# Optimization experiments

Hardware: AMD Instinct MI355X
Metric: run time of the kernel (lower is better)

Reference implementation:

```python
import jax, jax.numpy as jnp
import numpy as np

E = 600000
N = 50000
H = 128
OE = 256


def swish(v):
    return v * jax.nn.sigmoid(v)


def setup_inputs() -> dict:
    key = jax.random.key(0)
    ks = jax.random.split(key, 16)
    inp = {
        "x": jax.random.normal(ks[0], (E, H), dtype=jnp.float32),
        "rbf": jax.random.normal(ks[1], (E, 6), dtype=jnp.float32),
        "i": jax.random.randint(ks[2], (E,), 0, N, dtype=jnp.int32),
        "edge_index": jax.random.randint(ks[3], (2, E), 0, N, dtype=jnp.int32),
        "edge_weight": jax.random.uniform(ks[4], (E,), dtype=jnp.float32),
        "batch": jax.random.randint(ks[5], (N,), 0, 32, dtype=jnp.int32),
        "num_nodes": N,
        "W_rbf": jax.random.normal(ks[6], (H, 6), dtype=jnp.float32) * 0.2,
        "W_up": jax.random.normal(ks[7], (OE, H), dtype=jnp.float32) * (1.0 / np.sqrt(H)),
        "b_up": jnp.zeros((OE,), dtype=jnp.float32),
        "W_l1": jax.random.normal(ks[8], (OE, OE), dtype=jnp.float32) * (1.0 / np.sqrt(OE)),
        "b_l1": jnp.zeros((OE,), dtype=jnp.float32),
        "W_l2": jax.random.normal(ks[9], (OE, OE), dtype=jnp.float32) * (1.0 / np.sqrt(OE)),
        "b_l2": jnp.zeros((OE,), dtype=jnp.float32),
        "W_l3": jax.random.normal(ks[10], (OE, OE), dtype=jnp.float32) * (1.0 / np.sqrt(OE)),
        "b_l3": jnp.zeros((OE,), dtype=jnp.float32),
        "W_out": jax.random.normal(ks[11], (1, OE), dtype=jnp.float32) * (1.0 / np.sqrt(OE)),
        "W_w": jax.random.normal(ks[12], (1, H), dtype=jnp.float32) * (1.0 / np.sqrt(H)),
        "b_w": jnp.zeros((1,), dtype=jnp.float32),
    }
    return inp


def reference(x, rbf, i, edge_index, edge_weight, batch, num_nodes,
              W_rbf, W_up, b_up, W_l1, b_l1, W_l2, b_l2, W_l3, b_l3,
              W_out, W_w, b_w):
    # edge_index / edge_weight are unused in the original forward.
    # x = lin_rbf(rbf) * x  -> [E, H]
    xe = (rbf @ W_rbf.T) * x
    # scatter-add edges -> nodes: [N, H]
    xn = jax.ops.segment_sum(xe, i, num_segments=num_nodes)
    # energy head: alpha = w_lin(x) before lin_up
    alpha = xn @ W_w.T + b_w  # [N, 1]
    x2 = xn @ W_up.T + b_up   # [N, OE]
    for W, b in ((W_l1, b_l1), (W_l2, b_l2), (W_l3, b_l3)):
        x2 = swish(x2 @ W.T + b)
    out = (x2 @ W_out.T) * alpha  # [N, 1]
    return (out, batch)
```

## Files before the change

kernel.cpp:

```cpp
#include <hip/hip_runtime.h>
#include <hip/hip_bf16.h>
#include <math.h>

#define E_CNT 600000
#define N_CNT 50000
#define H_DIM 128
#define OE_DIM 256

typedef __attribute__((ext_vector_type(8))) short short8;
typedef __attribute__((ext_vector_type(4))) float f32x4;

#define WS_EIDS   0
#define WS_OFF    2400000
#define WS_CURS   2600008
#define WS_CNT    2800008
#define WS_WUP    3000016
#define WS_WL1    3065552
#define WS_WL2    3196624
#define WS_WL3    3327696
#define WS_TEXC   3500000
#define WS_BSUM   3700704
#define WS_BEXC   3701728

#define SCAN_NB 196
#define WCONV_NB 896

__global__ __launch_bounds__(256) void histwconv_kernel(
    const int* __restrict__ nid, int* __restrict__ counts,
    const float* __restrict__ Wup, const float* __restrict__ Wl1,
    const float* __restrict__ Wl2, const float* __restrict__ Wl3,
    ushort* __restrict__ dUp, ushort* __restrict__ dL1,
    ushort* __restrict__ dL2, ushort* __restrict__ dL3)
{
    if (blockIdx.x < WCONV_NB) {
        int d = blockIdx.x * 256 + threadIdx.x;
        const float* W;
        ushort* dst;
        int K;
        if (d < 32768)       { W = Wup; dst = dUp; K = 128; }
        else if (d < 98304)  { d -= 32768;  W = Wl1; dst = dL1; K = 256; }
        else if (d < 163840) { d -= 98304;  W = Wl2; dst = dL2; K = 256; }
        else                 { d -= 163840; W = Wl3; dst = dL3; K = 256; }
        int j = d & 7;
        int l = (d >> 3) & 63;
        int KS = K >> 5;
        int ks = (d >> 9) % KS;
        int ot = (d >> 9) / KS;
        int k = ks * 32 + ((l >> 4) << 3) + j;
        int o = ot * 16 + (l & 15);
        __hip_bfloat16 h = __float2bfloat16(W[o * K + k]);
        dst[d] = *(const ushort*)&h;
    } else {
        int nb = gridDim.x - WCONV_NB;
        for (int e = (blockIdx.x - WCONV_NB) * 256 + threadIdx.x; e < E_CNT;
             e += nb * 256)
            atomicAdd(&counts[nid[e]], 1);
    }
}

__global__ __launch_bounds__(256) void scanA_kernel(const int* __restrict__ counts,
                                                    int* __restrict__ texc,
                                                    int* __restrict__ bsum)
{
    __shared__ int s[256];
    const int t = threadIdx.x;
    const int i = blockIdx.x * 256 + t;
    int v = (i < N_CNT) ? counts[i] : 0;
    s[t] = v;
    __syncthreads();
    for (int off = 1; off < 256; off <<= 1) {
        int u = (t >= off) ? s[t - off] : 0;
        __syncthreads();
        s[t] += u;
        __syncthreads();
    }
    texc[i] = s[t] - v;
    if (t == 255) bsum[blockIdx.x] = s[255];
}

__global__ __launch_bounds__(256) void scanB_kernel(const int* __restrict__ bsum,
                                                    int* __restrict__ bexc)
{
    __shared__ int s[256];
    const int t = threadIdx.x;
    int v = (t < SCAN_NB) ? bsum[t] : 0;
    s[t] = v;
    __syncthreads();
    for (int off = 1; off < 256; off <<= 1) {
        int u = (t >= off) ? s[t - off] : 0;
        __syncthreads();
        s[t] += u;
        __syncthreads();
    }
    bexc[t] = s[t] - v;
}

__global__ __launch_bounds__(256) void scanC_kernel(const int* __restrict__ texc,
                                                    const int* __restrict__ bexc,
                                                    int* __restrict__ offs,
                                                    int* __restrict__ cursor)
{
    const int i = blockIdx.x * 256 + threadIdx.x;
    if (i < N_CNT) {
        int o = texc[i] + bexc[i >> 8];
        offs[i] = o;
        cursor[i] = o;
    }
    if (i == 0) offs[N_CNT] = E_CNT;
}

__global__ __launch_bounds__(256) void fill_kernel(const int* __restrict__ nid,
                                                   int* __restrict__ cursor,
                                                   int* __restrict__ eids)
{
    for (int e = blockIdx.x * 256 + threadIdx.x; e < E_CNT; e += gridDim.x * 256) {
        int slot = atomicAdd(&cursor[nid[e]], 1);
        eids[slot] = e;
    }
}

#define MB 32
#define PITCH 264
#define EMAX 640

template<int KS, bool SW>
__device__ __forceinline__ void layer(const ushort* __restrict__ Wsh,
                                      const float* __restrict__ bias,
                                      const ushort* in_s, ushort* out_s, int tid)
{
    const int w = tid >> 6, lane = tid & 63;
    const int l15 = lane & 15, lg = lane >> 4;

    f32x4 acc[2][2];
#pragma unroll
    for (int mi = 0; mi < 2; ++mi)
#pragma unroll
        for (int oi = 0; oi < 2; ++oi)
            acc[mi][oi] = (f32x4){0.f, 0.f, 0.f, 0.f};

#pragma unroll
    for (int ks = 0; ks < KS; ++ks) {
        short8 b0 = *(const short8*)(Wsh + (size_t)(((w * 2 + 0) * KS + ks) * 64 + lane) * 8);
        short8 b1 = *(const short8*)(Wsh + (size_t)(((w * 2 + 1) * KS + ks) * 64 + lane) * 8);
#pragma unroll
        for (int mi = 0; mi < 2; ++mi) {
            short8 a = *(const short8*)(in_s + (mi * 16 + l15) * PITCH + ks * 32 + lg * 8);
            acc[mi][0] = __builtin_amdgcn_mfma_f32_16x16x32_bf16(a, b0, acc[mi][0], 0, 0, 0);
            acc[mi][1] = __builtin_amdgcn_mfma_f32_16x16x32_bf16(a, b1, acc[mi][1], 0, 0, 0);
        }
    }

#pragma unroll
    for (int oi = 0; oi < 2; ++oi) {
        float bv = bias[(w * 2 + oi) * 16 + l15];
#pragma unroll
        for (int mi = 0; mi < 2; ++mi)
#pragma unroll
            for (int r = 0; r < 4; ++r) {
                float v = acc[mi][oi][r] + bv;
                if (SW) v = v / (1.f + __expf(-v));
                __hip_bfloat16 h = __float2bfloat16(v);
                out_s[(mi * 16 + lg * 4 + r) * PITCH + (w * 2 + oi) * 16 + l15] =
                    *(const ushort*)&h;
            }
    }
}

__global__ __launch_bounds__(512, 8) void fused_kernel(
    const float* __restrict__ x, const float* __restrict__ rbf,
    const int* __restrict__ offs, const int* __restrict__ eids,
    const float* __restrict__ W_rbf, const float* __restrict__ W_w,
    const float* __restrict__ b_w,
    const ushort* __restrict__ Wup, const ushort* __restrict__ Wl1,
    const ushort* __restrict__ Wl2, const ushort* __restrict__ Wl3,
    const float* __restrict__ b_up, const float* __restrict__ b_l1,
    const float* __restrict__ b_l2, const float* __restrict__ b_l3,
    const float* __restrict__ W_out, const int* __restrict__ batch,
    float* __restrict__ out)
{
    __shared__ ushort sA[MB * PITCH];
    __shared__ ushort sB[MB * PITCH];
    __shared__ int s_eids[EMAX];
    __shared__ int s_off[MB + 1];
    __shared__ float s_alpha[MB];

    const int tid = threadIdx.x;
    const int w = tid >> 6, lane = tid & 63;
    const int node0 = blockIdx.x * MB;

    if (tid < MB) {
        int node = node0 + tid;
        if (node < N_CNT) out[N_CNT + node] = (float)batch[node];
    }
    if (tid < MB + 1)
        s_off[tid] = offs[min(node0 + tid, N_CNT)];
    __syncthreads();

    const int s0 = s_off[0];
    const int tot = s_off[MB] - s0;
    const int nchunks = (tot + EMAX - 1) / EMAX;

    {
        const int half = lane >> 5;
        const int hb = (lane & 31) * 4;
        float wrb[4][6];
#pragma unroll
        for (int j = 0; j < 4; ++j)
#pragma unroll
            for (int k = 0; k < 6; ++k)
                wrb[j][k] = W_rbf[(hb + j) * 6 + k];
        float ww[4];
#pragma unroll
        for (int j = 0; j < 4; ++j) ww[j] = W_w[hb + j];
        const float bw = b_w[0];

        for (int c = 0; c < nchunks; ++c) {
            const int cs = c * EMAX;
            const int ce = min(cs + EMAX, tot);
            __syncthreads();
            for (int t = tid + cs; t < ce; t += 512) s_eids[t - cs] = eids[s0 + t];
            __syncthreads();

            for (int nl4 = 0; nl4 < 4; ++nl4) {
                const int nl = (w << 2) + nl4;
                const int ls = max(s_off[nl] - s0, cs);
                const int le = min(s_off[nl + 1] - s0, ce);
                float a0 = 0.f, a1 = 0.f, a2 = 0.f, a3 = 0.f;
                int i = ls;
                for (; i + 1 < le; i += 2) {
                    const int ee = s_eids[i - cs + half];
                    const float4 xv = *(const float4*)(x + (size_t)ee * H_DIM + hb);
                    const float2* rp = (const float2*)(rbf + (size_t)ee * 6);
                    const float2 r01 = rp[0], r23 = rp[1], r45 = rp[2];
                    float r[6] = {r01.x, r01.y, r23.x, r23.y, r45.x, r45.y};
                    float c0 = 0.f, c1 = 0.f, c2 = 0.f, c3 = 0.f;
#pragma unroll
                    for (int k = 0; k < 6; ++k) {
                        c0 = fmaf(r[k], wrb[0][k], c0);
                        c1 = fmaf(r[k], wrb[1][k], c1);
                        c2 = fmaf(r[k], wrb[2][k], c2);
                        c3 = fmaf(r[k], wrb[3][k], c3);
                    }
                    a0 = fmaf(c0, xv.x, a0);
                    a1 = fmaf(c1, xv.y, a1);
                    a2 = fmaf(c2, xv.z, a2);
                    a3 = fmaf(c3, xv.w, a3);
                }
                if (i < le && half == 0) {
                    const int ee = s_eids[i - cs];
                    const float4 xv = *(const float4*)(x + (size_t)ee * H_DIM + hb);
                    const float2* rp = (const float2*)(rbf + (size_t)ee * 6);
                    const float2 r01 = rp[0], r23 = rp[1], r45 = rp[2];
                    float r[6] = {r01.x, r01.y, r23.x, r23.y, r45.x, r45.y};
                    float c0 = 0.f, c1 = 0.f, c2 = 0.f, c3 = 0.f;
#pragma unroll
                    for (int k = 0; k < 6; ++k) {
                        c0 = fmaf(r[k], wrb[0][k], c0);
                        c1 = fmaf(r[k], wrb[1][k], c1);
                        c2 = fmaf(r[k], wrb[2][k], c2);
                        c3 = fmaf(r[k], wrb[3][k], c3);
                    }
                    a0 = fmaf(c0, xv.x, a0);
                    a1 = fmaf(c1, xv.y, a1);
                    a2 = fmaf(c2, xv.z, a2);
                    a3 = fmaf(c3, xv.w, a3);
                }

                a0 += __shfl_xor(a0, 32);
                a1 += __shfl_xor(a1, 32);
                a2 += __shfl_xor(a2, 32);
                a3 += __shfl_xor(a3, 32);

                if (half == 0) {
                    ushort4* dp = (ushort4*)(sA + nl * PITCH + hb);
                    if (c > 0) {
                        ushort4 old = *dp;
                        a0 += __bfloat162float(*(const __hip_bfloat16*)&old.x);
                        a1 += __bfloat162float(*(const __hip_bfloat16*)&old.y);
                        a2 += __bfloat162float(*(const __hip_bfloat16*)&old.z);
                        a3 += __bfloat162float(*(const __hip_bfloat16*)&old.w);
                    }
                    __hip_bfloat16 h0 = __float2bfloat16(a0), h1 = __float2bfloat16(a1);
                    __hip_bfloat16 h2 = __float2bfloat16(a2), h3 = __float2bfloat16(a3);
                    ushort4 pk;
                    pk.x = *(const ushort*)&h0;
                    pk.y = *(const ushort*)&h1;
                    pk.z = *(const ushort*)&h2;
                    pk.w = *(const ushort*)&h3;
                    *dp = pk;
                }

                float part = fmaf(a0, ww[0], fmaf(a1, ww[1], fmaf(a2, ww[2], a3 * ww[3])));
                part += __shfl_xor(part, 1);
                part += __shfl_xor(part, 2);
                part += __shfl_xor(part, 4);
                part += __shfl_xor(part, 8);
                part += __shfl_xor(part, 16);
                if (lane == 0) {
                    if (c > 0) s_alpha[nl] += part;
                    else       s_alpha[nl] = part + bw;
                }
            }
        }
    }
    __syncthreads();

    layer<4, false>(Wup, b_up, sA, sB, tid);
    __syncthreads();
    layer<8, true>(Wl1, b_l1, sB, sA, tid);
    __syncthreads();
    layer<8, true>(Wl2, b_l2, sA, sB, tid);
    __syncthreads();
    layer<8, true>(Wl3, b_l3, sB, sA, tid);
    __syncthreads();

    {
        int nl = tid >> 4, q = tid & 15;
        const ushort* rowp = sA + nl * PITCH + q * 16;
        float sum = 0.f;
#pragma unroll
        for (int o = 0; o < 16; ++o) {
            __hip_bfloat16 h = *(const __hip_bfloat16*)(rowp + o);
            sum = fmaf(__bfloat162float(h), W_out[q * 16 + o], sum);
        }
        sum += __shfl_xor(sum, 1);
        sum += __shfl_xor(sum, 2);
        sum += __shfl_xor(sum, 4);
        sum += __shfl_xor(sum, 8);
        int node = node0 + nl;
        if (q == 0 && node < N_CNT) out[node] = sum * s_alpha[nl];
    }
}

extern "C" void kernel_launch(void* const* d_in, const int* in_sizes, int n_in,
                              void* d_out, int out_size, void* d_ws, size_t ws_size,
                              hipStream_t stream)
{
    const float* x      = (const float*)d_in[0];
    const float* rbf    = (const float*)d_in[1];
    const int*   nid    = (const int*)d_in[2];
    const int*   batch  = (const int*)d_in[5];
    const float* W_rbf  = (const float*)d_in[7];
    const float* W_up   = (const float*)d_in[8];
    const float* b_up   = (const float*)d_in[9];
    const float* W_l1   = (const float*)d_in[10];
    const float* b_l1   = (const float*)d_in[11];
    const float* W_l2   = (const float*)d_in[12];
    const float* b_l2   = (const float*)d_in[13];
    const float* W_l3   = (const float*)d_in[14];
    const float* b_l3   = (const float*)d_in[15];
    const float* W_out  = (const float*)d_in[16];
    const float* W_w    = (const float*)d_in[17];
    const float* b_w    = (const float*)d_in[18];

    char* ws = (char*)d_ws;
    int*    eids   = (int*)(ws + WS_EIDS);
    int*    offs   = (int*)(ws + WS_OFF);
    int*    cursor = (int*)(ws + WS_CURS);
    int*    counts = (int*)(ws + WS_CNT);
    ushort* WupS   = (ushort*)(ws + WS_WUP);
    ushort* Wl1S   = (ushort*)(ws + WS_WL1);
    ushort* Wl2S   = (ushort*)(ws + WS_WL2);
    ushort* Wl3S   = (ushort*)(ws + WS_WL3);
    int*    texc   = (int*)(ws + WS_TEXC);
    int*    bsum   = (int*)(ws + WS_BSUM);
    int*    bexc   = (int*)(ws + WS_BEXC);
    float*  out    = (float*)d_out;

    hipMemsetAsync(counts, 0, N_CNT * sizeof(int), stream);
    histwconv_kernel<<<WCONV_NB + 1024, 256, 0, stream>>>(
        nid, counts, W_up, W_l1, W_l2, W_l3, WupS, Wl1S, Wl2S, Wl3S);
    scanA_kernel<<<SCAN_NB, 256, 0, stream>>>(counts, texc, bsum);
    scanB_kernel<<<1, 256, 0, stream>>>(bsum, bexc);
    scanC_kernel<<<SCAN_NB, 256, 0, stream>>>(texc, bexc, offs, cursor);
    fill_kernel<<<1024, 256, 0, stream>>>(nid, cursor, eids);

    fused_kernel<<<(N_CNT + MB - 1) / MB, 512, 0, stream>>>(
        x, rbf, offs, eids, W_rbf, W_w, b_w,
        WupS, Wl1S, Wl2S, Wl3S, b_up, b_l1, b_l2, b_l3, W_out, batch, out);
}
```

Baseline: 223.6 us.

## Merge scan kernels, prefetch next edge loads, relax fused kernel occupancy bound

Removes the single-block scanB kernel: each scanC block now sums the block totals before it with a shared-memory reduction, saving one launch and a serial dependency. The edge-gather loop in the fused kernel software-pipelines the x/rbf loads, fetching the next edge pair while computing the current one, to hide gather latency. The launch bounds minimum blocks drops from 8 to 4, so the compiler may use more registers for the prefetch buffers, at the risk of lower occupancy.

After: 228.6 us. +2.2%, slower.

```diff
diff --git a/kernel.cpp b/kernel.cpp
--- a/kernel.cpp
+++ b/kernel.cpp
@@ -20,7 +20,6 @@
 #define WS_WL3    3327696
 #define WS_TEXC   3500000
 #define WS_BSUM   3700704
-#define WS_BEXC   3701728
 
 #define SCAN_NB 196
 #define WCONV_NB 896
@@ -78,31 +77,24 @@
     if (t == 255) bsum[blockIdx.x] = s[255];
 }
 
-__global__ __launch_bounds__(256) void scanB_kernel(const int* __restrict__ bsum,
-                                                    int* __restrict__ bexc)
-{
-    __shared__ int s[256];
-    const int t = threadIdx.x;
-    int v = (t < SCAN_NB) ? bsum[t] : 0;
-    s[t] = v;
-    __syncthreads();
-    for (int off = 1; off < 256; off <<= 1) {
-        int u = (t >= off) ? s[t - off] : 0;
-        __syncthreads();
-        s[t] += u;
-        __syncthreads();
-    }
-    bexc[t] = s[t] - v;
-}
-
 __global__ __launch_bounds__(256) void scanC_kernel(const int* __restrict__ texc,
-                                                    const int* __restrict__ bexc,
+                                                    const int* __restrict__ bsum,
                                                     int* __restrict__ offs,
                                                     int* __restrict__ cursor)
 {
-    const int i = blockIdx.x * 256 + threadIdx.x;
+    __shared__ int red[256];
+    const int t = threadIdx.x;
+    int v = (t < (int)blockIdx.x && t < SCAN_NB) ? bsum[t] : 0;
+    red[t] = v;
+    __syncthreads();
+    for (int off = 128; off >= 1; off >>= 1) {
+        if (t < off) red[t] += red[t + off];
+        __syncthreads();
+    }
+    const int boff = red[0];
+    const int i = blockIdx.x * 256 + t;
     if (i < N_CNT) {
-        int o = texc[i] + bexc[i >> 8];
+        int o = texc[i] + boff;
         offs[i] = o;
         cursor[i] = o;
     }
@@ -166,7 +158,7 @@
     }
 }
 
-__global__ __launch_bounds__(512, 8) void fused_kernel(
+__global__ __launch_bounds__(512, 4) void fused_kernel(
     const float* __restrict__ x, const float* __restrict__ rbf,
     const int* __restrict__ offs, const int* __restrict__ eids,
     const float* __restrict__ W_rbf, const float* __restrict__ W_w,
@@ -226,13 +218,27 @@
                 const int ls = max(s_off[nl] - s0, cs);
                 const int le = min(s_off[nl + 1] - s0, ce);
                 float a0 = 0.f, a1 = 0.f, a2 = 0.f, a3 = 0.f;
+
                 int i = ls;
-                for (; i + 1 < le; i += 2) {
+                float4 xv_n = make_float4(0.f, 0.f, 0.f, 0.f);
+                float2 q0n = make_float2(0.f, 0.f), q1n = q0n, q2n = q0n;
+                if (i + 1 < le) {
                     const int ee = s_eids[i - cs + half];
-                    const float4 xv = *(const float4*)(x + (size_t)ee * H_DIM + hb);
+                    xv_n = *(const float4*)(x + (size_t)ee * H_DIM + hb);
                     const float2* rp = (const float2*)(rbf + (size_t)ee * 6);
-                    const float2 r01 = rp[0], r23 = rp[1], r45 = rp[2];
-                    float r[6] = {r01.x, r01.y, r23.x, r23.y, r45.x, r45.y};
+                    q0n = rp[0]; q1n = rp[1]; q2n = rp[2];
+                }
+                for (; i + 1 < le; ) {
+                    const float4 xv = xv_n;
+                    const float2 q0 = q0n, q1 = q1n, q2 = q2n;
+                    i += 2;
+                    if (i + 1 < le) {
+                        const int ee = s_eids[i - cs + half];
+                        xv_n = *(const float4*)(x + (size_t)ee * H_DIM + hb);
+                        const float2* rp = (const float2*)(rbf + (size_t)ee * 6);
+                        q0n = rp[0]; q1n = rp[1]; q2n = rp[2];
+                    }
+                    const float r[6] = {q0.x, q0.y, q1.x, q1.y, q2.x, q2.y};
                     float c0 = 0.f, c1 = 0.f, c2 = 0.f, c3 = 0.f;
 #pragma unroll
                     for (int k = 0; k < 6; ++k) {
@@ -250,8 +256,8 @@
                     const int ee = s_eids[i - cs];
                     const float4 xv = *(const float4*)(x + (size_t)ee * H_DIM + hb);
                     const float2* rp = (const float2*)(rbf + (size_t)ee * 6);
-                    const float2 r01 = rp[0], r23 = rp[1], r45 = rp[2];
-                    float r[6] = {r01.x, r01.y, r23.x, r23.y, r45.x, r45.y};
+                    const float2 q0 = rp[0], q1 = rp[1], q2 = rp[2];
+                    const float r[6] = {q0.x, q0.y, q1.x, q1.y, q2.x, q2.y};
                     float c0 = 0.f, c1 = 0.f, c2 = 0.f, c3 = 0.f;
 #pragma unroll
                     for (int k = 0; k < 6; ++k) {
@@ -364,15 +370,13 @@
     ushort* Wl3S   = (ushort*)(ws + WS_WL3);
     int*    texc   = (int*)(ws + WS_TEXC);
     int*    bsum   = (int*)(ws + WS_BSUM);
-    int*    bexc   = (int*)(ws + WS_BEXC);
     float*  out    = (float*)d_out;
 
     hipMemsetAsync(counts, 0, N_CNT * sizeof(int), stream);
     histwconv_kernel<<<WCONV_NB + 1024, 256, 0, stream>>>(
         nid, counts, W_up, W_l1, W_l2, W_l3, WupS, Wl1S, Wl2S, Wl3S);
     scanA_kernel<<<SCAN_NB, 256, 0, stream>>>(counts, texc, bsum);
-    scanB_kernel<<<1, 256, 0, stream>>>(bsum, bexc);
-    scanC_kernel<<<SCAN_NB, 256, 0, stream>>>(texc, bexc, offs, cursor);
+    scanC_kernel<<<SCAN_NB, 256, 0, stream>>>(texc, bsum, offs, cursor);
     fill_kernel<<<1024, 256, 0, stream>>>(nid, cursor, eids);
 
     fused_kernel<<<(N_CNT + MB - 1) / MB, 512, 0, stream>>>(
```
